# Kernel optimization log

Measured on AMD Instinct MI355X. Metric: run time of the kernel, lower is better.

The kernel has to match this reference:

```python
import jax, jax.numpy as jnp
import numpy as np

N_NODES = 100000
N_EDGES = 1600000
D_IN = 16
D_HID = 32   # 2 * out_channels
D_OUT = 16


def gcn_conv(h, src, dst, W, b, num_nodes):
    """PyG-style GCNConv: x' = D^{-1/2} (A+I) D^{-1/2} (x W) + b.
    src/dst already include self-loops."""
    h = h @ W                                   # [N, F_out] linear transform first
    deg = jnp.zeros((num_nodes,), h.dtype).at[dst].add(1.0)
    dinv = jax.lax.rsqrt(jnp.maximum(deg, 1.0))  # deg >= 1 due to self-loops
    norm = dinv[src] * dinv[dst]                # [E+N]
    msg = h[src] * norm[:, None]                # edge gather (memory-bound)
    out = jax.ops.segment_sum(msg, dst, num_segments=num_nodes)
    return out + b


def setup_inputs() -> dict:
    key = jax.random.key(0)
    k1, k2, k3, k4 = jax.random.split(key, 4)
    x = jnp.arange(N_NODES, dtype=jnp.int32)
    edge_index = jax.random.randint(k1, (2, N_EDGES), 0, N_NODES, dtype=jnp.int32)
    emb = jax.random.normal(k2, (N_NODES, D_IN), dtype=jnp.float32)
    W1 = jax.random.normal(k3, (D_IN, D_HID), dtype=jnp.float32) * (1.0 / np.sqrt(D_IN))
    b1 = jnp.zeros((D_HID,), jnp.float32)
    W2 = jax.random.normal(k4, (D_HID, D_OUT), dtype=jnp.float32) * (1.0 / np.sqrt(D_HID))
    b2 = jnp.zeros((D_OUT,), jnp.float32)
    return {"x": x, "edge_index": edge_index, "emb": emb,
            "W1": W1, "b1": b1, "W2": W2, "b2": b2}


def reference(x, edge_index, emb, W1, b1, W2, b2):
    num_nodes = emb.shape[0]
    # add self-loops once; reused by both conv layers
    loops = jnp.arange(num_nodes, dtype=edge_index.dtype)
    src = jnp.concatenate([edge_index[0], loops])
    dst = jnp.concatenate([edge_index[1], loops])

    h = emb[x]                                  # embedding lookup
    h = jax.nn.relu(gcn_conv(h, src, dst, W1, b1, num_nodes))
    # dropout is identity in eval mode (reference baseline)
    out = gcn_conv(h, src, dst, W2, b2, num_nodes)
    return out
```

## Files before the change

kernel.cpp:

```cpp
#include <hip/hip_runtime.h>


#define BS   256
#define BSBIG 1024
#define NBLK 256
#define BINSHIFT 8
#define BIN  256
#define MAXBINS 512
#define BINCAP 4608

union H2 { int i; _Float16 h[2]; };

__global__ __launch_bounds__(BSBIG) void k_hist(
    const int* __restrict__ dst, int E, int NBINS, int* __restrict__ histG) {
    __shared__ int h[MAXBINS];
    int t = threadIdx.x;
    for (int i = t; i < NBINS; i += BSBIG) h[i] = 0;
    __syncthreads();
    int E4 = E >> 2;
    const int4* d4 = (const int4*)dst;
    for (int i = blockIdx.x * BSBIG + t; i < E4; i += NBLK * BSBIG) {
        int4 d = d4[i];
        atomicAdd(&h[d.x >> BINSHIFT], 1);
        atomicAdd(&h[d.y >> BINSHIFT], 1);
        atomicAdd(&h[d.z >> BINSHIFT], 1);
        atomicAdd(&h[d.w >> BINSHIFT], 1);
    }
    if (blockIdx.x == 0 && t < (E & 3))
        atomicAdd(&h[dst[(E4 << 2) + t] >> BINSHIFT], 1);
    __syncthreads();
    for (int i = t; i < NBINS; i += BSBIG) histG[i * NBLK + blockIdx.x] = h[i];
}

__global__ void k_scanA(const int* __restrict__ in, int L,
                        int* __restrict__ partial, int* __restrict__ bsum) {
    __shared__ int s[BS];
    int t = threadIdx.x;
    int i = blockIdx.x * BS + t;
    int v = (i < L) ? in[i] : 0;
    s[t] = v;
    __syncthreads();
    for (int off = 1; off < BS; off <<= 1) {
        int add = (t >= off) ? s[t - off] : 0;
        __syncthreads();
        s[t] += add;
        __syncthreads();
    }
    if (i < L) partial[i] = s[t] - v;
    if (t == BS - 1) bsum[blockIdx.x] = s[BS - 1];
}

__global__ void k_scanB(const int* __restrict__ bsum, int nB, int* __restrict__ boff) {
    __shared__ int s[BS];
    int t = threadIdx.x;
    int PER = (nB + BS - 1) / BS;
    int loc[8];
    int base = t * PER;
    int sum = 0;
    for (int j = 0; j < PER && j < 8; j++) {
        int idx = base + j;
        int v = (idx < nB) ? bsum[idx] : 0;
        loc[j] = sum;
        sum += v;
    }
    s[t] = sum;
    __syncthreads();
    for (int off = 1; off < BS; off <<= 1) {
        int add = (t >= off) ? s[t - off] : 0;
        __syncthreads();
        s[t] += add;
        __syncthreads();
    }
    int ex = s[t] - sum;
    for (int j = 0; j < PER && j < 8; j++) {
        int idx = base + j;
        if (idx < nB) boff[idx] = ex + loc[j];
    }
}

__global__ __launch_bounds__(BSBIG) void k_binscatter(
    const int* __restrict__ src, const int* __restrict__ dst,
    int E, int NBINS, const int* __restrict__ partial,
    const int* __restrict__ boff, int* __restrict__ packed) {
    __shared__ int cur[MAXBINS];
    int t = threadIdx.x;
    for (int i = t; i < NBINS; i += BSBIG)
        cur[i] = partial[i * NBLK + blockIdx.x] + boff[i];
    __syncthreads();
    int E4 = E >> 2;
    const int4* s4 = (const int4*)src;
    const int4* d4 = (const int4*)dst;
    for (int i = blockIdx.x * BSBIG + t; i < E4; i += NBLK * BSBIG) {
        int4 s = s4[i];
        int4 d = d4[i];
        int p0 = atomicAdd(&cur[d.x >> BINSHIFT], 1);
        packed[p0] = s.x | ((d.x & (BIN - 1)) << 18);
        int p1 = atomicAdd(&cur[d.y >> BINSHIFT], 1);
        packed[p1] = s.y | ((d.y & (BIN - 1)) << 18);
        int p2 = atomicAdd(&cur[d.z >> BINSHIFT], 1);
        packed[p2] = s.z | ((d.z & (BIN - 1)) << 18);
        int p3 = atomicAdd(&cur[d.w >> BINSHIFT], 1);
        packed[p3] = s.w | ((d.w & (BIN - 1)) << 18);
    }
    if (blockIdx.x == 0 && t < (E & 3)) {
        int e = (E4 << 2) + t;
        int d = dst[e];
        int p = atomicAdd(&cur[d >> BINSHIFT], 1);
        packed[p] = src[e] | ((d & (BIN - 1)) << 18);
    }
}

__global__ void k_binsort(const int* __restrict__ packed,
                          const int* __restrict__ partial, const int* __restrict__ boff,
                          int NBINS, int N, int E,
                          const int* __restrict__ x, const float* __restrict__ emb,
                          const float* __restrict__ W1,
                          int* __restrict__ row_start, float* __restrict__ dinv,
                          int* __restrict__ col, _Float16* __restrict__ sig1) {
    __shared__ int buf[BINCAP];
    __shared__ int ldeg[BIN];
    __shared__ int lrs[BIN];
    __shared__ int cur[BIN];
    __shared__ float sW[512];
    int b = blockIdx.x;
    int t = threadIdx.x;
    int node0 = b << BINSHIFT;
    int e0 = partial[b * NBLK] + boff[b];
    int e1 = (b + 1 < NBINS) ? (partial[(b + 1) * NBLK] + boff[b + 1]) : E;
    int cnt = e1 - e0;
    bool fits = (cnt <= BINCAP);
    if (b == 0 && t == 0) row_start[N] = E;
    sW[t] = W1[t];
    sW[t + 256] = W1[t + 256];
    ldeg[t] = 0;
    if (fits)
        for (int i = t; i < cnt; i += BS) buf[i] = packed[e0 + i];
    __syncthreads();
    for (int i = t; i < cnt; i += BS) {
        int v = fits ? buf[i] : packed[e0 + i];
        atomicAdd(&ldeg[((unsigned)v >> 18) & (BIN - 1)], 1);
    }
    __syncthreads();
    lrs[t] = ldeg[t];
    __syncthreads();
    for (int off = 1; off < BIN; off <<= 1) {
        int add = (t >= off) ? lrs[t - off] : 0;
        __syncthreads();
        lrs[t] += add;
        __syncthreads();
    }
    int myDeg = ldeg[t];
    int ex = lrs[t] - myDeg;
    cur[t] = ex;
    int n = node0 + t;
    float di = rsqrtf((float)(myDeg + 1));
    if (n < N) {
        row_start[n] = e0 + ex;
        dinv[n] = di;
    }
    __syncthreads();
    for (int i = t; i < cnt; i += BS) {
        int v = fits ? buf[i] : packed[e0 + i];
        int pos = atomicAdd(&cur[((unsigned)v >> 18) & (BIN - 1)], 1);
        col[e0 + pos] = v & 0x3FFFF;
    }
    if (n < N) {
        const float4* er = (const float4*)(emb + (size_t)x[n] * 16);
        float4 ra = er[0], rb = er[1], rc = er[2], rd = er[3];
        float ev[16] = {ra.x, ra.y, ra.z, ra.w, rb.x, rb.y, rb.z, rb.w,
                        rc.x, rc.y, rc.z, rc.w, rd.x, rd.y, rd.z, rd.w};
        int4* s1o = (int4*)sig1;
        #pragma unroll
        for (int cq = 0; cq < 4; cq++) {
            H2 pk[4];
            #pragma unroll
            for (int dw = 0; dw < 4; dw++) {
                int c = cq * 8 + dw * 2;
                float acc0 = 0.f, acc1 = 0.f;
                #pragma unroll
                for (int k = 0; k < 16; k++) {
                    acc0 += ev[k] * sW[k * 32 + c];
                    acc1 += ev[k] * sW[k * 32 + c + 1];
                }
                pk[dw].h[0] = (_Float16)(acc0 * di);
                pk[dw].h[1] = (_Float16)(acc1 * di);
            }
            int4 pv;
            pv.x = pk[0].i; pv.y = pk[1].i; pv.z = pk[2].i; pv.w = pk[3].i;
            s1o[(size_t)n * 4 + cq] = pv;
        }
    }
}

__global__ __launch_bounds__(BS) void k_agg1mm2(
    const _Float16* __restrict__ sig1, const int* __restrict__ row_start,
    const float* __restrict__ dinv, const int* __restrict__ col,
    const float* __restrict__ b1, const float* __restrict__ W2,
    int N, _Float16* __restrict__ sig2) {
    __shared__ float hbuf[4][4][36];
    int t = threadIdx.x;
    int lane = t & 63;
    int wid = t >> 6;
    int g  = lane >> 4;
    int cd = lane & 15;
    int n = blockIdx.x * 16 + wid * 4 + g;
    int nld = (n < N) ? n : N - 1;
    int rs = row_start[nld];
    int re = row_start[nld + 1];
    int dn = (n < N) ? (re - rs) : 0;
    int dnm1 = (dn > 0) ? dn - 1 : 0;
    int dm = dn;
    dm = max(dm, __shfl_xor(dm, 16));
    dm = max(dm, __shfl_xor(dm, 32));
    float w2c[32];
    #pragma unroll
    for (int k = 0; k < 32; k++) w2c[k] = W2[k * 16 + cd];
    const int* s1i = (const int*)sig1;
    float a0 = 0.f, a1 = 0.f;
    int iters = (dm + 3) >> 2;
    int slot = cd & 3;
    int bidx = lane & 48;
    int colv = 0;
    if (iters > 0) {
        int idx = slot; if (idx > dnm1) idx = dnm1;
        colv = col[rs + idx];
    }
    for (int it = 0; it < iters; it++) {
        int e = it << 2;
        int coln = 0;
        if (it + 1 < iters) {
            int idx = e + 4 + slot; if (idx > dnm1) idx = dnm1;
            coln = col[rs + idx];
        }
        int s0 = __shfl(colv, bidx + 0);
        int s1 = __shfl(colv, bidx + 1);
        int s2 = __shfl(colv, bidx + 2);
        int s3 = __shfl(colv, bidx + 3);
        int u0 = s1i[s0 * 16 + cd];
        int u1 = s1i[s1 * 16 + cd];
        int u2 = s1i[s2 * 16 + cd];
        int u3 = s1i[s3 * 16 + cd];
        u0 = (e + 0 < dn) ? u0 : 0;
        u1 = (e + 1 < dn) ? u1 : 0;
        u2 = (e + 2 < dn) ? u2 : 0;
        u3 = (e + 3 < dn) ? u3 : 0;
        H2 p0, p1, p2, p3;
        p0.i = u0; p1.i = u1; p2.i = u2; p3.i = u3;
        a0 += ((float)p0.h[0] + (float)p1.h[0]) + ((float)p2.h[0] + (float)p3.h[0]);
        a1 += ((float)p0.h[1] + (float)p1.h[1]) + ((float)p2.h[1] + (float)p3.h[1]);
        colv = coln;
    }
    {
        H2 p; p.i = s1i[nld * 16 + cd];
        a0 += (float)p.h[0];
        a1 += (float)p.h[1];
    }
    float di = dinv[nld];
    float2 b = ((const float2*)b1)[cd];
    float h0 = fmaxf(a0 * di + b.x, 0.f);
    float h1 = fmaxf(a1 * di + b.y, 0.f);
    float* hb = hbuf[wid][g];
    *(float2*)&hb[2 * cd] = make_float2(h0, h1);
    float a = 0.f;
    #pragma unroll
    for (int k = 0; k < 32; k += 4) {
        float4 hv = *(const float4*)&hb[k];
        a = fmaf(hv.x, w2c[k],     a);
        a = fmaf(hv.y, w2c[k + 1], a);
        a = fmaf(hv.z, w2c[k + 2], a);
        a = fmaf(hv.w, w2c[k + 3], a);
    }
    if (n < N) sig2[(size_t)n * 16 + cd] = (_Float16)(a * di);
}

__global__ __launch_bounds__(BS) void k_agg2(
    const _Float16* __restrict__ sig2, const int* __restrict__ row_start,
    const float* __restrict__ dinv, const int* __restrict__ col,
    const float* __restrict__ b2, int N, float* __restrict__ out) {
    int t = threadIdx.x;
    int lane = t & 63;
    int g  = lane >> 4;
    int e2 = (lane >> 3) & 1;
    int cd = lane & 7;
    int n = blockIdx.x * 16 + (t >> 6) * 4 + g;
    int nld = (n < N) ? n : N - 1;
    int rs = row_start[nld];
    int re = row_start[nld + 1];
    int dn = (n < N) ? (re - rs) : 0;
    int dnm1 = (dn > 0) ? dn - 1 : 0;
    int dm = dn;
    dm = max(dm, __shfl_xor(dm, 16));
    dm = max(dm, __shfl_xor(dm, 32));
    const int* s2i = (const int*)sig2;
    float a0 = 0.f, a1 = 0.f;
    int iters = (dm + 7) >> 3;
    int slot = lane & 7;
    int bidx = lane & 48;
    int colv = 0;
    if (iters > 0) {
        int idx = slot; if (idx > dnm1) idx = dnm1;
        colv = col[rs + idx];
    }
    for (int it = 0; it < iters; it++) {
        int e = it << 3;
        int coln = 0;
        if (it + 1 < iters) {
            int idx = e + 8 + slot; if (idx > dnm1) idx = dnm1;
            coln = col[rs + idx];
        }
        #pragma unroll
        for (int j = 0; j < 4; j++) {
            int sl = 2 * j + e2;
            int sv = __shfl(colv, bidx + sl);
            int u = s2i[sv * 8 + cd];
            u = (e + sl < dn) ? u : 0;
            H2 p; p.i = u;
            a0 += (float)p.h[0];
            a1 += (float)p.h[1];
        }
        colv = coln;
    }
    a0 += __shfl_xor(a0, 8);
    a1 += __shfl_xor(a1, 8);
    {
        H2 p; p.i = s2i[nld * 8 + cd];
        a0 += (float)p.h[0];
        a1 += (float)p.h[1];
    }
    if (n < N && e2 == 0) {
        float di = dinv[nld];
        float2 b = ((const float2*)b2)[cd];
        float2 o;
        o.x = a0 * di + b.x;
        o.y = a1 * di + b.y;
        ((float2*)out)[(size_t)n * 8 + cd] = o;
    }
}

extern "C" void kernel_launch(void* const* d_in, const int* in_sizes, int n_in,
                              void* d_out, int out_size, void* d_ws, size_t ws_size,
                              hipStream_t stream) {
    const int*   x   = (const int*)d_in[0];
    const int*   ei  = (const int*)d_in[1];
    const float* emb = (const float*)d_in[2];
    const float* W1  = (const float*)d_in[3];
    const float* b1  = (const float*)d_in[4];
    const float* W2  = (const float*)d_in[5];
    const float* b2  = (const float*)d_in[6];
    float* out = (float*)d_out;

    const int N = in_sizes[0];
    const int E = in_sizes[1] / 2;
    const int* srcp = ei;
    const int* dstp = ei + E;
    const int NBINS = (N + BIN - 1) >> BINSHIFT;
    const int L = NBINS * NBLK;
    const int nB2 = (L + BS - 1) / BS;

    auto al = [](size_t b) { return (b + 255) & ~size_t(255); };
    char* w = (char*)d_ws;
    auto carve = [&](size_t bytes) {
        void* p = (void*)w;
        w += al(bytes);
        return p;
    };
    int*   row_start = (int*)carve((size_t)(N + 1) * 4);
    float* dinv      = (float*)carve((size_t)N * 4);
    int*   col       = (int*)carve((size_t)(E + 256) * 4);
    int*   histG     = (int*)carve((size_t)L * 4);
    int*   partial   = (int*)carve((size_t)L * 4);
    int*   bsum      = (int*)carve((size_t)nB2 * 4);
    int*   boff      = (int*)carve((size_t)nB2 * 4);
    int*   packed    = (int*)carve((size_t)E * 4);
    _Float16* sig1   = (_Float16*)carve((size_t)N * 32 * 2);
    _Float16* sig2   = (_Float16*)carve((size_t)N * 16 * 2);
    (void)ws_size; (void)n_in; (void)out_size;

    int gL = (L + BS - 1) / BS;
    k_hist<<<NBLK, BSBIG, 0, stream>>>(dstp, E, NBINS, histG);
    k_scanA<<<gL, BS, 0, stream>>>(histG, L, partial, bsum);
    k_scanB<<<1, BS, 0, stream>>>(bsum, nB2, boff);
    k_binscatter<<<NBLK, BSBIG, 0, stream>>>(srcp, dstp, E, NBINS, partial, boff,
                                             packed);
    k_binsort<<<NBINS, BS, 0, stream>>>(packed, partial, boff, NBINS, N, E,
                                        x, emb, W1, row_start, dinv, col, sig1);

    int gA = (N + 15) / 16;
    k_agg1mm2<<<gA, BS, 0, stream>>>(sig1, row_start, dinv, col, b1, W2, N, sig2);
    k_agg2<<<gA, BS, 0, stream>>>(sig2, row_start, dinv, col, b2, N, out);
}
```

Baseline: 155.9 us.

## Sort nodes by degree within bins and widen edge batches in aggregation kernels

The bin-sort kernel now builds a per-bin permutation of nodes ordered by descending degree, using a 64-bucket counting sort. Both aggregation kernels process nodes through this permutation, so the nodes sharing a wavefront have similar degrees and less time goes to lanes idling on the group's maximum degree. Each loop iteration now handles 8 edges per node in layer 1 and 16 in layer 2, which cuts loop overhead and puts more loads in flight. The cost is an extra perm array, one more indirection per node, and output writes that become scattered within each bin.

```diff
diff --git a/kernel.cpp b/kernel.cpp
--- a/kernel.cpp
+++ b/kernel.cpp
@@ -116,12 +116,14 @@
                           const int* __restrict__ x, const float* __restrict__ emb,
                           const float* __restrict__ W1,
                           int* __restrict__ row_start, float* __restrict__ dinv,
-                          int* __restrict__ col, _Float16* __restrict__ sig1) {
+                          int* __restrict__ col, _Float16* __restrict__ sig1,
+                          int* __restrict__ perm) {
     __shared__ int buf[BINCAP];
     __shared__ int ldeg[BIN];
     __shared__ int lrs[BIN];
     __shared__ int cur[BIN];
     __shared__ float sW[512];
+    __shared__ int dh[64], dco[64], dcur[64];
     int b = blockIdx.x;
     int t = threadIdx.x;
     int node0 = b << BINSHIFT;
@@ -133,6 +135,7 @@
     sW[t] = W1[t];
     sW[t + 256] = W1[t + 256];
     ldeg[t] = 0;
+    if (t < 64) dh[t] = 0;
     if (fits)
         for (int i = t; i < cnt; i += BS) buf[i] = packed[e0 + i];
     __syncthreads();
@@ -154,11 +157,27 @@
     cur[t] = ex;
     int n = node0 + t;
     float di = rsqrtf((float)(myDeg + 1));
+    int bucket = 63 - min(myDeg, 63);
     if (n < N) {
         row_start[n] = e0 + ex;
         dinv[n] = di;
-    }
-    __syncthreads();
+        atomicAdd(&dh[bucket], 1);
+    }
+    __syncthreads();
+    if (t < 64) dco[t] = dh[t];
+    __syncthreads();
+    for (int off = 1; off < 64; off <<= 1) {
+        int add = (t < 64 && t >= off) ? dco[t - off] : 0;
+        __syncthreads();
+        if (t < 64) dco[t] += add;
+        __syncthreads();
+    }
+    if (t < 64) dcur[t] = dco[t] - dh[t];
+    __syncthreads();
+    if (n < N) {
+        int pos = atomicAdd(&dcur[bucket], 1);
+        perm[node0 + pos] = n;
+    }
     for (int i = t; i < cnt; i += BS) {
         int v = fits ? buf[i] : packed[e0 + i];
         int pos = atomicAdd(&cur[((unsigned)v >> 18) & (BIN - 1)], 1);
@@ -195,19 +214,20 @@
 __global__ __launch_bounds__(BS) void k_agg1mm2(
     const _Float16* __restrict__ sig1, const int* __restrict__ row_start,
     const float* __restrict__ dinv, const int* __restrict__ col,
-    const float* __restrict__ b1, const float* __restrict__ W2,
-    int N, _Float16* __restrict__ sig2) {
+    const int* __restrict__ perm, const float* __restrict__ b1,
+    const float* __restrict__ W2, int N, _Float16* __restrict__ sig2) {
     __shared__ float hbuf[4][4][36];
     int t = threadIdx.x;
     int lane = t & 63;
     int wid = t >> 6;
     int g  = lane >> 4;
     int cd = lane & 15;
-    int n = blockIdx.x * 16 + wid * 4 + g;
-    int nld = (n < N) ? n : N - 1;
-    int rs = row_start[nld];
-    int re = row_start[nld + 1];
-    int dn = (n < N) ? (re - rs) : 0;
+    int m = blockIdx.x * 16 + wid * 4 + g;
+    int mld = (m < N) ? m : N - 1;
+    int n = perm[mld];
+    int rs = row_start[n];
+    int re = row_start[n + 1];
+    int dn = (m < N) ? (re - rs) : 0;
     int dnm1 = (dn > 0) ? dn - 1 : 0;
     int dm = dn;
     dm = max(dm, __shfl_xor(dm, 16));
@@ -217,8 +237,8 @@
     for (int k = 0; k < 32; k++) w2c[k] = W2[k * 16 + cd];
     const int* s1i = (const int*)sig1;
     float a0 = 0.f, a1 = 0.f;
-    int iters = (dm + 3) >> 2;
-    int slot = cd & 3;
+    int iters = (dm + 7) >> 3;
+    int slot = cd & 7;
     int bidx = lane & 48;
     int colv = 0;
     if (iters > 0) {
@@ -226,36 +246,51 @@
         colv = col[rs + idx];
     }
     for (int it = 0; it < iters; it++) {
-        int e = it << 2;
+        int e = it << 3;
         int coln = 0;
         if (it + 1 < iters) {
-            int idx = e + 4 + slot; if (idx > dnm1) idx = dnm1;
+            int idx = e + 8 + slot; if (idx > dnm1) idx = dnm1;
             coln = col[rs + idx];
         }
         int s0 = __shfl(colv, bidx + 0);
         int s1 = __shfl(colv, bidx + 1);
         int s2 = __shfl(colv, bidx + 2);
         int s3 = __shfl(colv, bidx + 3);
+        int s4 = __shfl(colv, bidx + 4);
+        int s5 = __shfl(colv, bidx + 5);
+        int s6 = __shfl(colv, bidx + 6);
+        int s7 = __shfl(colv, bidx + 7);
         int u0 = s1i[s0 * 16 + cd];
         int u1 = s1i[s1 * 16 + cd];
         int u2 = s1i[s2 * 16 + cd];
         int u3 = s1i[s3 * 16 + cd];
+        int u4 = s1i[s4 * 16 + cd];
+        int u5 = s1i[s5 * 16 + cd];
+        int u6 = s1i[s6 * 16 + cd];
+        int u7 = s1i[s7 * 16 + cd];
         u0 = (e + 0 < dn) ? u0 : 0;
         u1 = (e + 1 < dn) ? u1 : 0;
         u2 = (e + 2 < dn) ? u2 : 0;
         u3 = (e + 3 < dn) ? u3 : 0;
+        u4 = (e + 4 < dn) ? u4 : 0;
+        u5 = (e + 5 < dn) ? u5 : 0;
+        u6 = (e + 6 < dn) ? u6 : 0;
+        u7 = (e + 7 < dn) ? u7 : 0;
         H2 p0, p1, p2, p3;
         p0.i = u0; p1.i = u1; p2.i = u2; p3.i = u3;
         a0 += ((float)p0.h[0] + (float)p1.h[0]) + ((float)p2.h[0] + (float)p3.h[0]);
         a1 += ((float)p0.h[1] + (float)p1.h[1]) + ((float)p2.h[1] + (float)p3.h[1]);
+        p0.i = u4; p1.i = u5; p2.i = u6; p3.i = u7;
+        a0 += ((float)p0.h[0] + (float)p1.h[0]) + ((float)p2.h[0] + (float)p3.h[0]);
+        a1 += ((float)p0.h[1] + (float)p1.h[1]) + ((float)p2.h[1] + (float)p3.h[1]);
         colv = coln;
     }
     {
-        H2 p; p.i = s1i[nld * 16 + cd];
+        H2 p; p.i = s1i[n * 16 + cd];
         a0 += (float)p.h[0];
         a1 += (float)p.h[1];
     }
-    float di = dinv[nld];
+    float di = dinv[n];
     float2 b = ((const float2*)b1)[cd];
     float h0 = fmaxf(a0 * di + b.x, 0.f);
     float h1 = fmaxf(a1 * di + b.y, 0.f);
@@ -270,31 +305,33 @@
         a = fmaf(hv.z, w2c[k + 2], a);
         a = fmaf(hv.w, w2c[k + 3], a);
     }
-    if (n < N) sig2[(size_t)n * 16 + cd] = (_Float16)(a * di);
+    if (m < N) sig2[(size_t)n * 16 + cd] = (_Float16)(a * di);
 }
 
 __global__ __launch_bounds__(BS) void k_agg2(
     const _Float16* __restrict__ sig2, const int* __restrict__ row_start,
     const float* __restrict__ dinv, const int* __restrict__ col,
-    const float* __restrict__ b2, int N, float* __restrict__ out) {
+    const int* __restrict__ perm, const float* __restrict__ b2,
+    int N, float* __restrict__ out) {
     int t = threadIdx.x;
     int lane = t & 63;
     int g  = lane >> 4;
     int e2 = (lane >> 3) & 1;
     int cd = lane & 7;
-    int n = blockIdx.x * 16 + (t >> 6) * 4 + g;
-    int nld = (n < N) ? n : N - 1;
-    int rs = row_start[nld];
-    int re = row_start[nld + 1];
-    int dn = (n < N) ? (re - rs) : 0;
+    int m = blockIdx.x * 16 + (t >> 6) * 4 + g;
+    int mld = (m < N) ? m : N - 1;
+    int n = perm[mld];
+    int rs = row_start[n];
+    int re = row_start[n + 1];
+    int dn = (m < N) ? (re - rs) : 0;
     int dnm1 = (dn > 0) ? dn - 1 : 0;
     int dm = dn;
     dm = max(dm, __shfl_xor(dm, 16));
     dm = max(dm, __shfl_xor(dm, 32));
     const int* s2i = (const int*)sig2;
     float a0 = 0.f, a1 = 0.f;
-    int iters = (dm + 7) >> 3;
-    int slot = lane & 7;
+    int iters = (dm + 15) >> 4;
+    int slot = lane & 15;
     int bidx = lane & 48;
     int colv = 0;
     if (iters > 0) {
@@ -302,14 +339,14 @@
         colv = col[rs + idx];
     }
     for (int it = 0; it < iters; it++) {
-        int e = it << 3;
+        int e = it << 4;
         int coln = 0;
         if (it + 1 < iters) {
-            int idx = e + 8 + slot; if (idx > dnm1) idx = dnm1;
+            int idx = e + 16 + slot; if (idx > dnm1) idx = dnm1;
             coln = col[rs + idx];
         }
         #pragma unroll
-        for (int j = 0; j < 4; j++) {
+        for (int j = 0; j < 8; j++) {
             int sl = 2 * j + e2;
             int sv = __shfl(colv, bidx + sl);
             int u = s2i[sv * 8 + cd];
@@ -323,12 +360,12 @@
     a0 += __shfl_xor(a0, 8);
     a1 += __shfl_xor(a1, 8);
     {
-        H2 p; p.i = s2i[nld * 8 + cd];
+        H2 p; p.i = s2i[n * 8 + cd];
         a0 += (float)p.h[0];
         a1 += (float)p.h[1];
     }
-    if (n < N && e2 == 0) {
-        float di = dinv[nld];
+    if (m < N && e2 == 0) {
+        float di = dinv[n];
         float2 b = ((const float2*)b2)[cd];
         float2 o;
         o.x = a0 * di + b.x;
@@ -367,6 +404,7 @@
     int*   row_start = (int*)carve((size_t)(N + 1) * 4);
     float* dinv      = (float*)carve((size_t)N * 4);
     int*   col       = (int*)carve((size_t)(E + 256) * 4);
+    int*   perm      = (int*)carve((size_t)(N + 256) * 4);
     int*   histG     = (int*)carve((size_t)L * 4);
     int*   partial   = (int*)carve((size_t)L * 4);
     int*   bsum      = (int*)carve((size_t)nB2 * 4);
@@ -383,9 +421,11 @@
     k_binscatter<<<NBLK, BSBIG, 0, stream>>>(srcp, dstp, E, NBINS, partial, boff,
                                              packed);
     k_binsort<<<NBINS, BS, 0, stream>>>(packed, partial, boff, NBINS, N, E,
-                                        x, emb, W1, row_start, dinv, col, sig1);
+                                        x, emb, W1, row_start, dinv, col, sig1,
+                                        perm);
 
     int gA = (N + 15) / 16;
-    k_agg1mm2<<<gA, BS, 0, stream>>>(sig1, row_start, dinv, col, b1, W2, N, sig2);
-    k_agg2<<<gA, BS, 0, stream>>>(sig2, row_start, dinv, col, b2, N, out);
-}
+    k_agg1mm2<<<gA, BS, 0, stream>>>(sig1, row_start, dinv, col, perm, b1, W2,
+                                     N, sig2);
+    k_agg2<<<gA, BS, 0, stream>>>(sig2, row_start, dinv, col, perm, b2, N, out);
+}
```

Measured after the change: 160.8 us. +3.1%, slower.
